# Kernel tuning notes

Hardware: AMD Instinct MI355X
Metric: run time of the kernel (lower is better)

Reference implementation:

```python
import jax, jax.numpy as jnp
import numpy as np

_INF = -1e+30
N_HEAD, D_MODEL, D_HEAD = 16, 1024, 64
SCALE = 1.0 / float(np.sqrt(D_HEAD))
LN_EPS = 1e-5


def layer_norm(x, g, b):
    mu = jnp.mean(x, axis=-1, keepdims=True)
    var = jnp.mean(jnp.square(x - mu), axis=-1, keepdims=True)
    return (x - mu) * jax.lax.rsqrt(var + LN_EPS) * g + b


def setup_inputs() -> dict:
    key = jax.random.key(0)
    k_h, k_m, k_q, k_k, k_v, k_o = jax.random.split(key, 6)
    B, S = 2, 2048
    h = jax.random.normal(k_h, (B, S, D_MODEL), dtype=jnp.float32)
    attn_mask = jax.random.randint(k_m, (B, S), 0, 2, dtype=jnp.int32)
    # torch Linear weights: [out_features, in_features], init N(0, scale)
    q_w = jax.random.normal(k_q, (N_HEAD * D_HEAD, D_MODEL), dtype=jnp.float32) * SCALE
    k_w = jax.random.normal(k_k, (N_HEAD * D_HEAD, D_MODEL), dtype=jnp.float32) * SCALE
    v_w = jax.random.normal(k_v, (N_HEAD * D_HEAD, D_MODEL), dtype=jnp.float32) * SCALE
    o_w = jax.random.normal(k_o, (D_MODEL, N_HEAD * D_HEAD), dtype=jnp.float32) * SCALE
    ln_g = jnp.ones((D_MODEL,), dtype=jnp.float32)
    ln_b = jnp.zeros((D_MODEL,), dtype=jnp.float32)
    return {"h": h, "attn_mask": attn_mask, "q_w": q_w, "k_w": k_w,
            "v_w": v_w, "o_w": o_w, "ln_g": ln_g, "ln_b": ln_b}


def reference(h, attn_mask, q_w, k_w, v_w, o_w, ln_g, ln_b):
    B, S, _ = h.shape
    # mems=None -> c == h; pre_lnorm=False
    head_q = (h @ q_w.T).reshape(B, S, N_HEAD, D_HEAD)
    head_k = (h @ k_w.T).reshape(B, S, N_HEAD, D_HEAD)
    head_v = (h @ v_w.T).reshape(B, S, N_HEAD, D_HEAD)
    # scores [b, i(q), j(k), n]
    attn_score = jnp.einsum('bind,bjnd->bijn', head_q, head_k) * SCALE
    mask = (attn_mask == 0)[:, None, :, None]  # [b,1,j,1]
    attn_score = jnp.where(mask, _INF, attn_score)
    attn_prob = jax.nn.softmax(attn_score, axis=2)
    attn_vec = jnp.einsum('bijn,bjnd->bind', attn_prob, head_v)
    attn_vec = attn_vec.reshape(B, S, N_HEAD * D_HEAD)
    attn_out = attn_vec @ o_w.T
    output = h + attn_out  # dropout=0 -> identity
    return layer_norm(output, ln_g, ln_b)  # post-lnorm
```

## Files before the change

kernel.cpp:

```cpp
#include <hip/hip_runtime.h>
#include <hip/hip_bf16.h>

typedef __attribute__((ext_vector_type(8))) _Float16 hfx8;
typedef __attribute__((ext_vector_type(16))) float fx16;
typedef __attribute__((ext_vector_type(2))) __fp16 fp16x2;
typedef __attribute__((ext_vector_type(4))) float fx4;
typedef __attribute__((ext_vector_type(4))) unsigned short usx4;
typedef __attribute__((ext_vector_type(8))) unsigned short usx8;
typedef __attribute__((ext_vector_type(2))) unsigned int ux2;

#define LOG2E 1.44269504f

__device__ __forceinline__ unsigned short f2h(float f) {
  union { _Float16 h; unsigned short u; } c;
  c.h = (_Float16)f;
  return c.u;
}

__device__ __forceinline__ void async16(const void* g, void* l) {
  __builtin_amdgcn_global_load_lds(
      (const __attribute__((address_space(1))) void*)g,
      (__attribute__((address_space(3))) void*)l, 16, 0, 0);
}

__global__ __launch_bounds__(256)
void cvth(const float* __restrict__ s, unsigned short* __restrict__ d) {
  int i = (blockIdx.x * 256 + threadIdx.x) * 4;
  fx4 v = *(const fx4*)(s + i);
  usx4 o;
  o[0] = f2h(v[0]); o[1] = f2h(v[1]); o[2] = f2h(v[2]); o[3] = f2h(v[3]);
  *(usx4*)(d + i) = o;
}

__global__ __launch_bounds__(256)
void cvtw(const float* __restrict__ s0, const float* __restrict__ s1,
          const float* __restrict__ s2, const float* __restrict__ s3,
          unsigned short* __restrict__ d0, unsigned short* __restrict__ d1,
          unsigned short* __restrict__ d2, unsigned short* __restrict__ d3) {
  const int y = blockIdx.y;
  const float* s = (y == 0) ? s0 : (y == 1) ? s1 : (y == 2) ? s2 : s3;
  unsigned short* d = (y == 0) ? d0 : (y == 1) ? d1 : (y == 2) ? d2 : d3;
  int i = (blockIdx.x * 256 + threadIdx.x) * 4;
  fx4 v = *(const fx4*)(s + i);
  usx4 o;
  o[0] = f2h(v[0]); o[1] = f2h(v[1]); o[2] = f2h(v[2]); o[3] = f2h(v[3]);
  *(usx4*)(d + i) = o;
}

__global__ __launch_bounds__(256)
void maskscan(const int* __restrict__ mask, int* __restrict__ src, int* __restrict__ cnt) {
  const int b = blockIdx.x;
  const int tid = threadIdx.x;
  const int base = b * 2048 + tid * 8;
  int m[8];
  int s = 0;
#pragma unroll
  for (int e = 0; e < 8; ++e) { m[e] = mask[base + e] ? 1 : 0; s += m[e]; }
  const int lane = tid & 63, wv = tid >> 6;
  int inc = s;
#pragma unroll
  for (int off = 1; off < 64; off <<= 1) {
    int t = __shfl_up(inc, off);
    if (lane >= off) inc += t;
  }
  __shared__ int wsum[4];
  if (lane == 63) wsum[wv] = inc;
  __syncthreads();
  int wvoff = 0;
#pragma unroll
  for (int k = 0; k < 4; ++k)
    if (k < wv) wvoff += wsum[k];
  int run = wvoff + inc - s;
#pragma unroll
  for (int e = 0; e < 8; ++e) {
    if (m[e]) { src[b * 2048 + run] = tid * 8 + e; ++run; }
  }
  if (tid == 255) cnt[b] = run;
}

__global__ __launch_bounds__(256, 2)
void gemm_qkv(const unsigned short* __restrict__ A,
              const unsigned short* __restrict__ Wq,
              const unsigned short* __restrict__ Wk,
              const unsigned short* __restrict__ Wv,
              const int* __restrict__ src, const int* __restrict__ cnt,
              unsigned short* __restrict__ Qf, unsigned short* __restrict__ Kf,
              unsigned short* __restrict__ Vt) {
  __shared__ unsigned short As[2][128 * 64];
  __shared__ unsigned short Bs[2][128 * 64];
  const int tid = threadIdx.x;
  const int w = tid >> 6, ln = tid & 63;
  const int bid = blockIdx.x;
  const int wg = (bid & 7) * 96 + (bid >> 3);
  const int mt = wg & 31;
  const int by = wg >> 5;
  const int sel = by >> 3;
  const int nt = by & 7;
  const unsigned short* W = (sel == 0) ? Wq : ((sel == 1) ? Wk : Wv);
  const int n0 = nt * 128;
  const int wr = w >> 1, wc = w & 1;

  const int lr = ln >> 3;
  const int scg = (ln & 7) ^ lr;

  const int bI = mt >> 4;
  const int r0 = (mt & 15) * 128;
  int cnt_b = 0;
  const unsigned short* Arow[4];
  if (sel == 0) {
    const int m0 = mt * 128;
#pragma unroll
    for (int ii = 0; ii < 4; ++ii)
      Arow[ii] = A + (size_t)(m0 + w * 32 + ii * 8 + lr) * 1024 + scg * 8;
  } else {
    cnt_b = cnt[bI];
    if (r0 >= cnt_b) return;
#pragma unroll
    for (int ii = 0; ii < 4; ++ii) {
      int r = r0 + w * 32 + ii * 8 + lr;
      r = (r < cnt_b) ? r : (cnt_b - 1);
      Arow[ii] = A + (size_t)(bI * 2048 + src[bI * 2048 + r]) * 1024 + scg * 8;
    }
  }
  const unsigned short* Bsrc = W + (size_t)(n0 + w * 32 + lr) * 1024 + scg * 8;

  fx4 acc[4][4] = {};

#define G_STAGE(KT, BI_)                                                       \
  {                                                                            \
    _Pragma("unroll") for (int i = 0; i < 4; ++i) {                            \
      async16(Arow[i] + (KT) * 64, &As[BI_][(w * 32 + i * 8) * 64]);           \
      async16(Bsrc + (size_t)i * 8 * 1024 + (KT) * 64, &Bs[BI_][(w * 32 + i * 8) * 64]); \
    }                                                                          \
  }

  G_STAGE(0, 0);
  for (int kt = 0; kt < 16; ++kt) {
    const int cur = kt & 1;
    __syncthreads();
    if (kt < 15) G_STAGE(kt + 1, cur ^ 1);
#pragma unroll
    for (int kk = 0; kk < 2; ++kk) {
      const int kg = kk * 4 + (ln >> 4);
      hfx8 af[4], bfr[4];
#pragma unroll
      for (int mi = 0; mi < 4; ++mi) {
        int row = wr * 64 + mi * 16 + (ln & 15);
        af[mi] = *(const hfx8*)&As[cur][row * 64 + ((kg ^ (row & 7)) * 8)];
      }
#pragma unroll
      for (int ni = 0; ni < 4; ++ni) {
        int row = wc * 64 + ni * 16 + (ln & 15);
        bfr[ni] = *(const hfx8*)&Bs[cur][row * 64 + ((kg ^ (row & 7)) * 8)];
      }
#pragma unroll
      for (int mi = 0; mi < 4; ++mi)
#pragma unroll
        for (int ni = 0; ni < 4; ++ni)
          acc[mi][ni] = __builtin_amdgcn_mfma_f32_16x16x32_f16(af[mi], bfr[ni], acc[mi][ni], 0, 0, 0);
    }
  }
#undef G_STAGE
  const int cb = n0 + wc * 64 + (ln & 15);
  const int rloc = wr * 64 + ((ln >> 4) << 2);
  if (sel == 0) {
    const int m0 = mt * 128;
#pragma unroll
    for (int mi = 0; mi < 4; ++mi)
#pragma unroll
      for (int ni = 0; ni < 4; ++ni)
#pragma unroll
        for (int j = 0; j < 4; ++j)
          Qf[(size_t)(m0 + rloc + mi * 16 + j) * 1024 + cb + ni * 16] = f2h(acc[mi][ni][j] * 0.125f);
  } else if (sel == 1) {
#pragma unroll
    for (int mi = 0; mi < 4; ++mi)
#pragma unroll
      for (int ni = 0; ni < 4; ++ni)
#pragma unroll
        for (int j = 0; j < 4; ++j)
          Kf[(size_t)(bI * 2048 + r0 + rloc + mi * 16 + j) * 1024 + cb + ni * 16] = f2h(acc[mi][ni][j]);
  } else {
#pragma unroll
    for (int mi = 0; mi < 4; ++mi)
#pragma unroll
      for (int ni = 0; ni < 4; ++ni) {
        int c = cb + ni * 16;
        int h2 = (c >> 6) & 15, d2 = c & 63;
        usx4 pk;
#pragma unroll
        for (int j = 0; j < 4; ++j) pk[j] = f2h(acc[mi][ni][j]);
        *(usx4*)&Vt[((size_t)(bI * 16 + h2) * 64 + d2) * 2048 + r0 + rloc + mi * 16] = pk;
      }
  }
}

__global__ __launch_bounds__(256, 2)
void gemm_o(const unsigned short* __restrict__ A,
            const unsigned short* __restrict__ W,
            float* __restrict__ O) {
  __shared__ unsigned short As[2][128 * 64];
  __shared__ unsigned short Bs[2][128 * 64];
  const int tid = threadIdx.x;
  const int w = tid >> 6, ln = tid & 63;
  const int mt = blockIdx.x, nt = blockIdx.y;
  const int m0 = mt * 128, n0 = nt * 128;
  const int wr = w >> 1, wc = w & 1;
  fx4 acc[4][4] = {};
  const int lr = ln >> 3;
  const int scg = (ln & 7) ^ lr;
  const unsigned short* Asrc = A + (size_t)(m0 + w * 32 + lr) * 1024 + scg * 8;
  const unsigned short* Bsrc = W + (size_t)(n0 + w * 32 + lr) * 1024 + scg * 8;

#define G_STAGE(KT, BI)                                                        \
  {                                                                            \
    _Pragma("unroll") for (int i = 0; i < 4; ++i) {                            \
      async16(Asrc + (size_t)i * 8 * 1024 + (KT) * 64, &As[BI][(w * 32 + i * 8) * 64]); \
      async16(Bsrc + (size_t)i * 8 * 1024 + (KT) * 64, &Bs[BI][(w * 32 + i * 8) * 64]); \
    }                                                                          \
  }

  G_STAGE(0, 0);
  for (int kt = 0; kt < 16; ++kt) {
    const int cur = kt & 1;
    __syncthreads();
    if (kt < 15) G_STAGE(kt + 1, cur ^ 1);
#pragma unroll
    for (int kk = 0; kk < 2; ++kk) {
      const int kg = kk * 4 + (ln >> 4);
      hfx8 af[4], bfr[4];
#pragma unroll
      for (int mi = 0; mi < 4; ++mi) {
        int row = wr * 64 + mi * 16 + (ln & 15);
        af[mi] = *(const hfx8*)&As[cur][row * 64 + ((kg ^ (row & 7)) * 8)];
      }
#pragma unroll
      for (int ni = 0; ni < 4; ++ni) {
        int row = wc * 64 + ni * 16 + (ln & 15);
        bfr[ni] = *(const hfx8*)&Bs[cur][row * 64 + ((kg ^ (row & 7)) * 8)];
      }
#pragma unroll
      for (int mi = 0; mi < 4; ++mi)
#pragma unroll
        for (int ni = 0; ni < 4; ++ni)
          acc[mi][ni] = __builtin_amdgcn_mfma_f32_16x16x32_f16(af[mi], bfr[ni], acc[mi][ni], 0, 0, 0);
    }
  }
#undef G_STAGE
  const int cb = n0 + wc * 64 + (ln & 15);
  const int rb = m0 + wr * 64 + ((ln >> 4) << 2);
#pragma unroll
  for (int mi = 0; mi < 4; ++mi)
#pragma unroll
    for (int ni = 0; ni < 4; ++ni)
#pragma unroll
      for (int j = 0; j < 4; ++j)
        O[(size_t)(rb + mi * 16 + j) * 1024 + cb + ni * 16] = acc[mi][ni][j];
}

__global__ __launch_bounds__(256, 2)
void attn_fwd(const unsigned short* __restrict__ Qf,
              const unsigned short* __restrict__ Kf,
              const unsigned short* __restrict__ Vt,
              const int* __restrict__ cnt,
              unsigned short* __restrict__ Ov) {
  __shared__ __align__(16) unsigned short smem[32768];
  unsigned short (*Ks)[8192] = (unsigned short (*)[8192])(smem);
  unsigned short (*Vs)[8192] = (unsigned short (*)[8192])(smem + 16384);
  unsigned short* eb = smem;

  const int tid = threadIdx.x;
  const int w = tid >> 6, ln = tid & 63;
  const int bid = blockIdx.x;
  const int wg = (bid & 7) * 64 + (bid >> 3);
  const int qt = wg & 15, h = (wg >> 4) & 15, b = wg >> 8;
  const int l31 = ln & 31, h5 = ln >> 5;
  const int q = qt * 128 + w * 32 + l31;

  const int cnt_b = cnt[b];
  const int ntile = (cnt_b + 127) >> 7;

  hfx8 qb[4];
  {
    const unsigned short* qp = Qf + (size_t)(b * 2048 + q) * 1024 + h * 64 + h5 * 8;
    qb[0] = *(const hfx8*)(qp);
    qb[1] = *(const hfx8*)(qp + 16);
    qb[2] = *(const hfx8*)(qp + 32);
    qb[3] = *(const hfx8*)(qp + 48);
  }

  fx16 o0 = {}, o1 = {};
  float mrow = -INFINITY, lrow = 0.f;

#define A_STAGE(KT, BI)                                                          \
  {                                                                              \
    _Pragma("unroll") for (int ii = 0; ii < 4; ++ii) {                           \
      int krow = w * 32 + ii * 8 + (ln >> 3);                                    \
      async16(Kf + ((size_t)(b * 2048 + (KT) * 128 + krow)) * 1024 + h * 64 +    \
                  (((ln & 7) ^ (ln >> 3)) * 8),                                  \
              &Ks[BI][(w * 4 + ii) * 512]);                                      \
      int vswz = (ii * 4 + (ln >> 4)) & 7;                                       \
      int vrow = w * 16 + ii * 4 + (ln >> 4);                                    \
      async16(Vt + ((size_t)((b * 16 + h) * 64 + vrow)) * 2048 + (KT) * 128 +    \
                  (((ln & 15) ^ vswz) * 8),                                      \
              &Vs[BI][(w * 4 + ii) * 512]);                                      \
    }                                                                            \
  }

  A_STAGE(0, 0);
  for (int kt = 0; kt < ntile; ++kt) {
    const int cur = kt & 1;
    __syncthreads();
    if (kt + 1 < ntile) A_STAGE(kt + 1, cur ^ 1);
    const bool lastt = (kt == ntile - 1);

    fx16 sArr[4];
#pragma unroll
    for (int kb = 0; kb < 4; ++kb) {
      fx16 z = {};
      if (lastt) {
#pragma unroll
        for (int r = 0; r < 16; ++r) {
          int crow = (r & 3) + 8 * (r >> 2) + 4 * h5;
          int key = kt * 128 + kb * 32 + crow;
          z[r] = (key < cnt_b) ? 0.0f : -1e30f;
        }
      }
#pragma unroll
      for (int dc = 0; dc < 4; ++dc) {
        int row = kb * 32 + l31;
        int slot = (dc * 2 + h5) ^ (l31 & 7);
        hfx8 a = *(const hfx8*)&Ks[cur][row * 64 + slot * 8];
        z = __builtin_amdgcn_mfma_f32_32x32x16_f16(a, qb[dc], z, 0, 0, 0);
      }
      sArr[kb] = z;
    }

    float tm = -INFINITY;
#pragma unroll
    for (int kb = 0; kb < 4; ++kb)
#pragma unroll
      for (int r = 0; r < 16; ++r) tm = fmaxf(tm, sArr[kb][r]);
    {
      auto t = __builtin_amdgcn_permlane32_swap(__float_as_uint(tm), __float_as_uint(tm), false, false);
      tm = fmaxf(__uint_as_float(t[0]), __uint_as_float(t[1]));
    }
    if (!__all(tm <= mrow + 8.0f)) {
      float mn = fmaxf(mrow, tm);
      float fac = exp2f((mrow - mn) * LOG2E);
      mrow = mn;
      lrow *= fac;
#pragma unroll
      for (int r = 0; r < 16; ++r) { o0[r] *= fac; o1[r] *= fac; }
    }
    const float nm2 = -mrow * LOG2E;
    float psum = 0.f;
    unsigned int pk[4][8];
#pragma unroll
    for (int kb = 0; kb < 4; ++kb) {
#pragma unroll
      for (int j = 0; j < 8; ++j) {
        float pa = exp2f(fmaf(sArr[kb][2 * j], LOG2E, nm2));
        float pb = exp2f(fmaf(sArr[kb][2 * j + 1], LOG2E, nm2));
        psum += pa + pb;
        union { fp16x2 h; unsigned int u; } rr;
        rr.h = __builtin_amdgcn_cvt_pkrtz(pa, pb);
        pk[kb][j] = rr.u;
      }
    }
    {
      auto t = __builtin_amdgcn_permlane32_swap(__float_as_uint(psum), __float_as_uint(psum), false, false);
      psum = __uint_as_float(t[0]) + __uint_as_float(t[1]);
    }
    lrow += psum;

#pragma unroll
    for (int kc = 0; kc < 8; ++kc) {
      const int kbq = kc >> 1;
      const int jb = (kc & 1) * 4;
      auto r0 = __builtin_amdgcn_permlane32_swap(pk[kbq][jb], pk[kbq][jb + 2], false, false);
      auto r1 = __builtin_amdgcn_permlane32_swap(pk[kbq][jb + 1], pk[kbq][jb + 3], false, false);
      union { unsigned int u[4]; hfx8 v; } B_;
      B_.u[0] = (unsigned int)r0[0];
      B_.u[1] = (unsigned int)r1[0];
      B_.u[2] = (unsigned int)r0[1];
      B_.u[3] = (unsigned int)r1[1];
      int slot = (kc * 2 + h5) ^ (l31 & 7);
      hfx8 va0 = *(const hfx8*)&Vs[cur][(l31) * 128 + slot * 8];
      o0 = __builtin_amdgcn_mfma_f32_32x32x16_f16(va0, B_.v, o0, 0, 0, 0);
      hfx8 va1 = *(const hfx8*)&Vs[cur][(32 + l31) * 128 + slot * 8];
      o1 = __builtin_amdgcn_mfma_f32_32x32x16_f16(va1, B_.v, o1, 0, 0, 0);
    }
  }
#undef A_STAGE

  __syncthreads();
  float inv = 1.0f / lrow;
  const int ql = w * 32 + l31;
#pragma unroll
  for (int db = 0; db < 2; ++db) {
#pragma unroll
    for (int r4 = 0; r4 < 4; ++r4) {
      float v0 = (db ? o1[4 * r4] : o0[4 * r4]) * inv;
      float v1 = (db ? o1[4 * r4 + 1] : o0[4 * r4 + 1]) * inv;
      float v2 = (db ? o1[4 * r4 + 2] : o0[4 * r4 + 2]) * inv;
      float v3 = (db ? o1[4 * r4 + 3] : o0[4 * r4 + 3]) * inv;
      union { fp16x2 h; unsigned int u; } pa_, pb_;
      pa_.h = __builtin_amdgcn_cvt_pkrtz(v0, v1);
      pb_.h = __builtin_amdgcn_cvt_pkrtz(v2, v3);
      ux2 tw; tw[0] = pa_.u; tw[1] = pb_.u;
      int d_base = db * 32 + 8 * r4 + 4 * h5;
      *(ux2*)&eb[ql * 88 + d_base] = tw;
    }
  }
  __syncthreads();
#pragma unroll
  for (int pass = 0; pass < 4; ++pass) {
    int idx = pass * 256 + tid;
    int qq = idx >> 3, slot = idx & 7;
    usx8 vv = *(const usx8*)&eb[qq * 88 + slot * 8];
    *(usx8*)&Ov[(size_t)(b * 2048 + qt * 128 + qq) * 1024 + h * 64 + slot * 8] = vv;
  }
}

__global__ __launch_bounds__(256)
void lnk(const float* __restrict__ h, const float* __restrict__ ao,
         const float* __restrict__ g, const float* __restrict__ bb,
         float* __restrict__ out) {
  const int row = blockIdx.x;
  const int tid = threadIdx.x;
  const size_t base = (size_t)row * 1024 + tid * 4;
  fx4 x = *(const fx4*)(h + base);
  fx4 a = *(const fx4*)(ao + base);
  x = x + a;
  float s = x[0] + x[1] + x[2] + x[3];
  float q = x[0] * x[0] + x[1] * x[1] + x[2] * x[2] + x[3] * x[3];
#pragma unroll
  for (int mm = 1; mm < 64; mm <<= 1) {
    s += __shfl_xor(s, mm);
    q += __shfl_xor(q, mm);
  }
  __shared__ float rs[4], rq[4];
  if ((tid & 63) == 0) { rs[tid >> 6] = s; rq[tid >> 6] = q; }
  __syncthreads();
  s = rs[0] + rs[1] + rs[2] + rs[3];
  q = rq[0] + rq[1] + rq[2] + rq[3];
  float mu = s * (1.0f / 1024.0f);
  float var = q * (1.0f / 1024.0f) - mu * mu;
  float rstd = rsqrtf(var + 1e-5f);
  fx4 gg = *(const fx4*)(g + tid * 4);
  fx4 bv = *(const fx4*)(bb + tid * 4);
  fx4 ov;
#pragma unroll
  for (int k = 0; k < 4; ++k) ov[k] = (x[k] - mu) * rstd * gg[k] + bv[k];
  *(fx4*)(out + base) = ov;
}

extern "C" void kernel_launch(void* const* d_in, const int* in_sizes, int n_in,
                              void* d_out, int out_size, void* d_ws, size_t ws_size,
                              hipStream_t stream) {
  const float* h = (const float*)d_in[0];
  const int* msk = (const int*)d_in[1];
  const float* qw = (const float*)d_in[2];
  const float* kw = (const float*)d_in[3];
  const float* vw = (const float*)d_in[4];
  const float* ow = (const float*)d_in[5];
  const float* lng = (const float*)d_in[6];
  const float* lnb = (const float*)d_in[7];
  float* out = (float*)d_out;
  char* ws = (char*)d_ws;

  const size_t MB = 1u << 20;
  unsigned short* h16 = (unsigned short*)(ws + 0 * MB);
  unsigned short* w16q = (unsigned short*)(ws + 8 * MB);
  unsigned short* w16k = (unsigned short*)(ws + 10 * MB);
  unsigned short* w16v = (unsigned short*)(ws + 12 * MB);
  unsigned short* w16o = (unsigned short*)(ws + 14 * MB);
  unsigned short* Qf  = (unsigned short*)(ws + 16 * MB);
  unsigned short* Kf  = (unsigned short*)(ws + 24 * MB);
  unsigned short* Vtb = (unsigned short*)(ws + 32 * MB);
  unsigned short* Av  = (unsigned short*)(ws + 40 * MB);
  float* Ao = (float*)(ws + 48 * MB);
  int* srcIdx = (int*)(ws + 48 * MB);
  int* cnt    = (int*)(ws + 48 * MB + 16384);

  cvth<<<dim3(4096), 256, 0, stream>>>(h, h16);
  cvtw<<<dim3(1024, 4), 256, 0, stream>>>(qw, kw, vw, ow, w16q, w16k, w16v, w16o);
  maskscan<<<dim3(2), 256, 0, stream>>>(msk, srcIdx, cnt);

  gemm_qkv<<<dim3(768), 256, 0, stream>>>(h16, w16q, w16k, w16v, srcIdx, cnt, Qf, Kf, Vtb);
  attn_fwd<<<dim3(512), 256, 0, stream>>>(Qf, Kf, Vtb, cnt, Av);
  gemm_o<<<dim3(32, 8), 256, 0, stream>>>(Av, w16o, Ao);
  lnk<<<dim3(4096), 256, 0, stream>>>(h, Ao, lng, lnb, out);
}
```

Baseline: 124.4 us.

## Single-buffer GEMM shared tiles and raise occupancy to four blocks per CU

Both projection GEMM kernels drop their LDS double buffer and use one A and one B tile. Each K step now loads, syncs, computes and syncs again, and the launch bound goes from 2 to 4 blocks per multiprocessor. The aim is to hide load latency through more resident blocks instead of in-kernel prefetch. This gives up load/compute overlap inside a block and adds a barrier per iteration, and the higher launch bound may squeeze registers for the 64-float accumulator.

```diff
diff --git a/kernel.cpp b/kernel.cpp
--- a/kernel.cpp
+++ b/kernel.cpp
@@ -78,7 +78,7 @@
   if (tid == 255) cnt[b] = run;
 }
 
-__global__ __launch_bounds__(256, 2)
+__global__ __launch_bounds__(256, 4)
 void gemm_qkv(const unsigned short* __restrict__ A,
               const unsigned short* __restrict__ Wq,
               const unsigned short* __restrict__ Wk,
@@ -86,8 +86,8 @@
               const int* __restrict__ src, const int* __restrict__ cnt,
               unsigned short* __restrict__ Qf, unsigned short* __restrict__ Kf,
               unsigned short* __restrict__ Vt) {
-  __shared__ unsigned short As[2][128 * 64];
-  __shared__ unsigned short Bs[2][128 * 64];
+  __shared__ unsigned short As[128 * 64];
+  __shared__ unsigned short Bs[128 * 64];
   const int tid = threadIdx.x;
   const int w = tid >> 6, ln = tid & 63;
   const int bid = blockIdx.x;
@@ -126,19 +126,13 @@
 
   fx4 acc[4][4] = {};
 
-#define G_STAGE(KT, BI_)                                                       \
-  {                                                                            \
-    _Pragma("unroll") for (int i = 0; i < 4; ++i) {                            \
-      async16(Arow[i] + (KT) * 64, &As[BI_][(w * 32 + i * 8) * 64]);           \
-      async16(Bsrc + (size_t)i * 8 * 1024 + (KT) * 64, &Bs[BI_][(w * 32 + i * 8) * 64]); \
-    }                                                                          \
-  }
-
-  G_STAGE(0, 0);
   for (int kt = 0; kt < 16; ++kt) {
-    const int cur = kt & 1;
+#pragma unroll
+    for (int i = 0; i < 4; ++i) {
+      async16(Arow[i] + kt * 64, &As[(w * 32 + i * 8) * 64]);
+      async16(Bsrc + (size_t)i * 8 * 1024 + kt * 64, &Bs[(w * 32 + i * 8) * 64]);
+    }
     __syncthreads();
-    if (kt < 15) G_STAGE(kt + 1, cur ^ 1);
 #pragma unroll
     for (int kk = 0; kk < 2; ++kk) {
       const int kg = kk * 4 + (ln >> 4);
@@ -146,12 +140,12 @@
 #pragma unroll
       for (int mi = 0; mi < 4; ++mi) {
         int row = wr * 64 + mi * 16 + (ln & 15);
-        af[mi] = *(const hfx8*)&As[cur][row * 64 + ((kg ^ (row & 7)) * 8)];
+        af[mi] = *(const hfx8*)&As[row * 64 + ((kg ^ (row & 7)) * 8)];
       }
 #pragma unroll
       for (int ni = 0; ni < 4; ++ni) {
         int row = wc * 64 + ni * 16 + (ln & 15);
-        bfr[ni] = *(const hfx8*)&Bs[cur][row * 64 + ((kg ^ (row & 7)) * 8)];
+        bfr[ni] = *(const hfx8*)&Bs[row * 64 + ((kg ^ (row & 7)) * 8)];
       }
 #pragma unroll
       for (int mi = 0; mi < 4; ++mi)
@@ -159,8 +153,8 @@
         for (int ni = 0; ni < 4; ++ni)
           acc[mi][ni] = __builtin_amdgcn_mfma_f32_16x16x32_f16(af[mi], bfr[ni], acc[mi][ni], 0, 0, 0);
     }
-  }
-#undef G_STAGE
+    __syncthreads();
+  }
   const int cb = n0 + wc * 64 + (ln & 15);
   const int rloc = wr * 64 + ((ln >> 4) << 2);
   if (sel == 0) {
@@ -195,12 +189,12 @@
   }
 }
 
-__global__ __launch_bounds__(256, 2)
+__global__ __launch_bounds__(256, 4)
 void gemm_o(const unsigned short* __restrict__ A,
             const unsigned short* __restrict__ W,
             float* __restrict__ O) {
-  __shared__ unsigned short As[2][128 * 64];
-  __shared__ unsigned short Bs[2][128 * 64];
+  __shared__ unsigned short As[128 * 64];
+  __shared__ unsigned short Bs[128 * 64];
   const int tid = threadIdx.x;
   const int w = tid >> 6, ln = tid & 63;
   const int mt = blockIdx.x, nt = blockIdx.y;
@@ -212,19 +206,13 @@
   const unsigned short* Asrc = A + (size_t)(m0 + w * 32 + lr) * 1024 + scg * 8;
   const unsigned short* Bsrc = W + (size_t)(n0 + w * 32 + lr) * 1024 + scg * 8;
 
-#define G_STAGE(KT, BI)                                                        \
-  {                                                                            \
-    _Pragma("unroll") for (int i = 0; i < 4; ++i) {                            \
-      async16(Asrc + (size_t)i * 8 * 1024 + (KT) * 64, &As[BI][(w * 32 + i * 8) * 64]); \
-      async16(Bsrc + (size_t)i * 8 * 1024 + (KT) * 64, &Bs[BI][(w * 32 + i * 8) * 64]); \
-    }                                                                          \
-  }
-
-  G_STAGE(0, 0);
   for (int kt = 0; kt < 16; ++kt) {
-    const int cur = kt & 1;
+#pragma unroll
+    for (int i = 0; i < 4; ++i) {
+      async16(Asrc + (size_t)i * 8 * 1024 + kt * 64, &As[(w * 32 + i * 8) * 64]);
+      async16(Bsrc + (size_t)i * 8 * 1024 + kt * 64, &Bs[(w * 32 + i * 8) * 64]);
+    }
     __syncthreads();
-    if (kt < 15) G_STAGE(kt + 1, cur ^ 1);
 #pragma unroll
     for (int kk = 0; kk < 2; ++kk) {
       const int kg = kk * 4 + (ln >> 4);
@@ -232,12 +220,12 @@
 #pragma unroll
       for (int mi = 0; mi < 4; ++mi) {
         int row = wr * 64 + mi * 16 + (ln & 15);
-        af[mi] = *(const hfx8*)&As[cur][row * 64 + ((kg ^ (row & 7)) * 8)];
+        af[mi] = *(const hfx8*)&As[row * 64 + ((kg ^ (row & 7)) * 8)];
       }
 #pragma unroll
       for (int ni = 0; ni < 4; ++ni) {
         int row = wc * 64 + ni * 16 + (ln & 15);
-        bfr[ni] = *(const hfx8*)&Bs[cur][row * 64 + ((kg ^ (row & 7)) * 8)];
+        bfr[ni] = *(const hfx8*)&Bs[row * 64 + ((kg ^ (row & 7)) * 8)];
       }
 #pragma unroll
       for (int mi = 0; mi < 4; ++mi)
@@ -245,8 +233,8 @@
         for (int ni = 0; ni < 4; ++ni)
           acc[mi][ni] = __builtin_amdgcn_mfma_f32_16x16x32_f16(af[mi], bfr[ni], acc[mi][ni], 0, 0, 0);
     }
-  }
-#undef G_STAGE
+    __syncthreads();
+  }
   const int cb = n0 + wc * 64 + (ln & 15);
   const int rb = m0 + wr * 64 + ((ln >> 4) << 2);
 #pragma unroll
```

Measured after the change: 113.2 us. -9.0%, faster.
